# Performance work log

Measured on AMD Instinct MI355X. Metric: run time of the kernel, lower is better.

Reference implementation:

```python
import jax, jax.numpy as jnp
import numpy as np


def _gcn_layer(ann, adj, Wa, ba, W2, b2):
    # ann: [B,N,F], adj: [B,E,N,N], Wa: [E,F,U], ba: [E,U], W2: [F,U], b2: [U]
    # per-edge-type linear, fused as one batched einsum -> [B,E,N,U]
    h = jnp.einsum('bnf,efu->benu', ann, Wa) + ba[None, :, None, :]
    # adjacency matmul per edge type: [B,E,N,N] @ [B,E,N,U]
    h = jnp.einsum('benm,bemu->benu', adj, h)
    # sum over edge types + residual linear + activation (tanh)
    out = h.sum(axis=1) + jnp.einsum('bnf,fu->bnu', ann, W2) + b2
    return jnp.tanh(out)


def setup_inputs() -> dict:
    key = jax.random.key(0)
    ks = jax.random.split(key, 10)
    B, N, F, E, U = 32, 1024, 32, 4, 32
    s = 1.0 / np.sqrt(F)
    s1 = 1.0 / np.sqrt(F + U)
    return {
        'n_tensor': jax.random.normal(ks[0], (B, N, F), dtype=jnp.float32),
        'adj_tensor': jax.random.uniform(ks[1], (B, E, N, N), dtype=jnp.float32),
        'W_adj0': jax.random.normal(ks[2], (E, F, U), dtype=jnp.float32) * s,
        'b_adj0': jax.random.normal(ks[3], (E, U), dtype=jnp.float32) * s,
        'W2_0': jax.random.normal(ks[4], (F, U), dtype=jnp.float32) * s,
        'b2_0': jax.random.normal(ks[5], (U,), dtype=jnp.float32) * s,
        'W_adj1': jax.random.normal(ks[6], (E, F + U, U), dtype=jnp.float32) * s1,
        'b_adj1': jax.random.normal(ks[7], (E, U), dtype=jnp.float32) * s1,
        'W2_1': jax.random.normal(ks[8], (F + U, U), dtype=jnp.float32) * s1,
        'b2_1': jax.random.normal(ks[9], (U,), dtype=jnp.float32) * s1,
    }


def reference(n_tensor, adj_tensor, W_adj0, b_adj0, W2_0, b2_0,
              W_adj1, b_adj1, W2_1, b2_1):
    # layer 0: h_tensor is None -> annotations = n_tensor
    h = _gcn_layer(n_tensor, adj_tensor, W_adj0, b_adj0, W2_0, b2_0)
    # layer 1: annotations = cat(n_tensor, hidden)
    ann1 = jnp.concatenate([n_tensor, h], axis=-1)
    h = _gcn_layer(ann1, adj_tensor, W_adj1, b_adj1, W2_1, b2_1)
    return h
```

## Files before the change

### kernel.cpp

```cpp
#include <hip/hip_runtime.h>
#include <math.h>

#define Bb 32
#define Nn 1024
#define Ee 4
#define Uu 32

template <int F, int FA>
__global__ __launch_bounds__(128) void pre_kernel(
    const float* __restrict__ annA, const float* __restrict__ annB,
    const float* __restrict__ Wa, const float* __restrict__ ba,
    const float* __restrict__ W2, const float* __restrict__ b2,
    float* __restrict__ hpre_t, float* __restrict__ res)
{
    __shared__ float wlds[5 * F * Uu];
    __shared__ float blds[5 * Uu];
    const int tid = threadIdx.x;
    for (int i = tid; i < 4 * F * Uu; i += 128) wlds[i] = Wa[i];
    for (int i = tid; i < F * Uu; i += 128) wlds[4 * F * Uu + i] = W2[i];
    for (int i = tid; i < 4 * Uu; i += 128) blds[i] = ba[i];
    for (int i = tid; i < Uu; i += 128) blds[4 * Uu + i] = b2[i];
    __syncthreads();

    const int g = blockIdx.x * 128 + tid;
    const int b = g >> 10;
    const int n = g & 1023;

    float4 a4[F / 4];
    {
        const float4* rA = (const float4*)(annA + (size_t)g * FA);
#pragma unroll
        for (int i = 0; i < FA / 4; ++i) a4[i] = rA[i];
        if constexpr (F > FA) {
            const float4* rB = (const float4*)(annB + (size_t)g * (F - FA));
#pragma unroll
            for (int i = 0; i < (F - FA) / 4; ++i) a4[FA / 4 + i] = rB[i];
        }
    }

    for (int e = 0; e < 5; ++e) {
        float4 acc[8];
        const float4* bb = (const float4*)(blds + e * Uu);
#pragma unroll
        for (int uq = 0; uq < 8; ++uq) acc[uq] = bb[uq];
        const float4* w4 = (const float4*)wlds + (size_t)e * F * 8;
#pragma unroll
        for (int f4 = 0; f4 < F / 4; ++f4) {
            const float4 av = a4[f4];
#pragma unroll
            for (int c = 0; c < 4; ++c) {
                const float s = (c == 0) ? av.x : (c == 1) ? av.y : (c == 2) ? av.z : av.w;
#pragma unroll
                for (int uq = 0; uq < 8; ++uq) {
                    const float4 w = w4[(f4 * 4 + c) * 8 + uq];
                    acc[uq].x = fmaf(s, w.x, acc[uq].x);
                    acc[uq].y = fmaf(s, w.y, acc[uq].y);
                    acc[uq].z = fmaf(s, w.z, acc[uq].z);
                    acc[uq].w = fmaf(s, w.w, acc[uq].w);
                }
            }
        }
        if (e < 4) {
            float* dst = hpre_t + ((size_t)(b * 4 + e) * Uu) * Nn + n;
#pragma unroll
            for (int uq = 0; uq < 8; ++uq) {
                dst[(uq * 4 + 0) * Nn] = acc[uq].x;
                dst[(uq * 4 + 1) * Nn] = acc[uq].y;
                dst[(uq * 4 + 2) * Nn] = acc[uq].z;
                dst[(uq * 4 + 3) * Nn] = acc[uq].w;
            }
        } else {
            float4* dst = (float4*)(res + (size_t)g * Uu);
#pragma unroll
            for (int uq = 0; uq < 8; ++uq) dst[uq] = acc[uq];
        }
    }
}

__global__ __launch_bounds__(256) void gcn_main_kernel(
    const float* __restrict__ adj,
    const float* __restrict__ hpre_t,
    const float* __restrict__ res,
    float* __restrict__ out)
{
    __shared__ float hbuf[2][Uu * 64];

    const int bid = blockIdx.x;
    const int swz = (bid & 7) * 128 + (bid >> 3);
    const int b = swz >> 5;
    const int n0 = (swz & 31) * 32;
    const int tid = threadIdx.x;
    const int w = tid >> 6;
    const int lane = tid & 63;
    const int gu = lane >> 4;
    const int ms = lane & 15;
    const int wrow = n0 + w * 8;

    float acc[8][8];
#pragma unroll
    for (int r = 0; r < 8; ++r)
#pragma unroll
        for (int j = 0; j < 8; ++j) acc[r][j] = 0.f;

    const float* adjb = adj + (size_t)b * Ee * Nn * Nn;
    const float* hpb = hpre_t + (size_t)b * Ee * Uu * Nn;

    const int fi0 = tid, fi1 = tid + 256;
    const int su0 = fi0 >> 4, sm0 = fi0 & 15;
    const int su1 = fi1 >> 4, sm1 = fi1 & 15;

    float4 hstage0 = *(const float4*)(hpb + (size_t)su0 * Nn + sm0 * 4);
    float4 hstage1 = *(const float4*)(hpb + (size_t)su1 * Nn + sm1 * 4);

    for (int it = 0; it < 64; ++it) {
        const int e = it >> 4, c = it & 15;
        float* hb = hbuf[it & 1];

        const float* arow = adjb + ((size_t)e * Nn + wrow) * Nn + c * 64 + ms * 4;
        float4 av[8];
#pragma unroll
        for (int r = 0; r < 8; ++r) av[r] = *(const float4*)(arow + (size_t)r * Nn);

        ((float4*)hb)[fi0] = hstage0;
        ((float4*)hb)[fi1] = hstage1;

        if (it < 63) {
            const int e2 = (it + 1) >> 4, c2 = (it + 1) & 15;
            const float* hc = hpb + (size_t)e2 * Uu * Nn + c2 * 64;
            hstage0 = *(const float4*)(hc + (size_t)su0 * Nn + sm0 * 4);
            hstage1 = *(const float4*)(hc + (size_t)su1 * Nn + sm1 * 4);
        }
        __syncthreads();

#pragma unroll
        for (int j = 0; j < 8; ++j) {
            const float4 h = *(const float4*)(hb + (gu * 8 + j) * 64 + ms * 4);
#pragma unroll
            for (int r = 0; r < 8; ++r) {
                float t = fmaf(av[r].x, h.x, acc[r][j]);
                t = fmaf(av[r].y, h.y, t);
                t = fmaf(av[r].z, h.z, t);
                acc[r][j] = fmaf(av[r].w, h.w, t);
            }
        }
    }

#pragma unroll
    for (int r = 0; r < 8; ++r)
#pragma unroll
        for (int j = 0; j < 8; ++j) {
            float v = acc[r][j];
            v += __shfl_xor(v, 1);
            v += __shfl_xor(v, 2);
            v += __shfl_xor(v, 4);
            v += __shfl_xor(v, 8);
            acc[r][j] = v;
        }

#pragma unroll
    for (int r = 0; r < 8; ++r) {
        if (ms == r) {
            const int n = wrow + r;
            const float* rp = res + ((size_t)b * Nn + n) * Uu + gu * 8;
            float* op = out + ((size_t)b * Nn + n) * Uu + gu * 8;
            const float4 r0 = *(const float4*)(rp);
            const float4 r1 = *(const float4*)(rp + 4);
            float4 o0, o1;
            o0.x = tanhf(acc[r][0] + r0.x);
            o0.y = tanhf(acc[r][1] + r0.y);
            o0.z = tanhf(acc[r][2] + r0.z);
            o0.w = tanhf(acc[r][3] + r0.w);
            o1.x = tanhf(acc[r][4] + r1.x);
            o1.y = tanhf(acc[r][5] + r1.y);
            o1.z = tanhf(acc[r][6] + r1.z);
            o1.w = tanhf(acc[r][7] + r1.w);
            *(float4*)(op) = o0;
            *(float4*)(op + 4) = o1;
        }
    }
}

extern "C" void kernel_launch(void* const* d_in, const int* in_sizes, int n_in,
                              void* d_out, int out_size, void* d_ws, size_t ws_size,
                              hipStream_t stream)
{
    const float* n_tensor = (const float*)d_in[0];
    const float* adj      = (const float*)d_in[1];
    const float* W_adj0   = (const float*)d_in[2];
    const float* b_adj0   = (const float*)d_in[3];
    const float* W2_0     = (const float*)d_in[4];
    const float* b2_0     = (const float*)d_in[5];
    const float* W_adj1   = (const float*)d_in[6];
    const float* b_adj1   = (const float*)d_in[7];
    const float* W2_1     = (const float*)d_in[8];
    const float* b2_1     = (const float*)d_in[9];
    float* outp = (float*)d_out;

    float* ws   = (float*)d_ws;
    float* hpre = ws;
    float* resb = ws + (size_t)4 * 1024 * 1024;
    float* h0   = ws + (size_t)5 * 1024 * 1024;

    pre_kernel<32, 32><<<256, 128, 0, stream>>>(n_tensor, nullptr, W_adj0, b_adj0,
                                                W2_0, b2_0, hpre, resb);
    gcn_main_kernel<<<1024, 256, 0, stream>>>(adj, hpre, resb, h0);

    pre_kernel<64, 32><<<256, 128, 0, stream>>>(n_tensor, h0, W_adj1, b_adj1,
                                                W2_1, b2_1, hpre, resb);
    gcn_main_kernel<<<1024, 256, 0, stream>>>(adj, hpre, resb, outp);
}
```

Baseline: 496.3 us.

## Double-buffer adjacency loads in registers and split pre-kernel by edge type

The main GCN kernel now prefetches the next chunk's adjacency rows into an alternate register set (adjA/adjB ping-pong) while computing on the current one. It replaces __syncthreads with an explicit LDS waitcnt, a raw barrier and a sched_barrier, aiming to hide global load latency behind the FMAs. The pre-kernel is split across a second grid dimension, one block column per edge type plus the residual, with 256 threads. This gives more parallel blocks and smaller shared memory, at the cost of reloading the annotations five times. The extra adjacency register buffer raises register pressure and may reduce occupancy.

```diff
diff --git a/kernel.cpp b/kernel.cpp
--- a/kernel.cpp
+++ b/kernel.cpp
@@ -7,22 +7,23 @@
 #define Uu 32
 
 template <int F, int FA>
-__global__ __launch_bounds__(128) void pre_kernel(
+__global__ __launch_bounds__(256) void pre_kernel(
     const float* __restrict__ annA, const float* __restrict__ annB,
     const float* __restrict__ Wa, const float* __restrict__ ba,
     const float* __restrict__ W2, const float* __restrict__ b2,
     float* __restrict__ hpre_t, float* __restrict__ res)
 {
-    __shared__ float wlds[5 * F * Uu];
-    __shared__ float blds[5 * Uu];
+    const int e = blockIdx.y;
+    __shared__ float wlds[F * Uu];
+    __shared__ float blds[Uu];
     const int tid = threadIdx.x;
-    for (int i = tid; i < 4 * F * Uu; i += 128) wlds[i] = Wa[i];
-    for (int i = tid; i < F * Uu; i += 128) wlds[4 * F * Uu + i] = W2[i];
-    for (int i = tid; i < 4 * Uu; i += 128) blds[i] = ba[i];
-    for (int i = tid; i < Uu; i += 128) blds[4 * Uu + i] = b2[i];
+    const float* wsrc = (e < 4) ? (Wa + (size_t)e * F * Uu) : W2;
+    const float* bsrc = (e < 4) ? (ba + (size_t)e * Uu) : b2;
+    for (int i = tid; i < F * Uu; i += 256) wlds[i] = wsrc[i];
+    if (tid < Uu) blds[tid] = bsrc[tid];
     __syncthreads();
 
-    const int g = blockIdx.x * 128 + tid;
+    const int g = blockIdx.x * 256 + tid;
     const int b = g >> 10;
     const int n = g & 1023;
 
@@ -38,42 +39,40 @@
         }
     }
 
-    for (int e = 0; e < 5; ++e) {
-        float4 acc[8];
-        const float4* bb = (const float4*)(blds + e * Uu);
-#pragma unroll
-        for (int uq = 0; uq < 8; ++uq) acc[uq] = bb[uq];
-        const float4* w4 = (const float4*)wlds + (size_t)e * F * 8;
-#pragma unroll
-        for (int f4 = 0; f4 < F / 4; ++f4) {
-            const float4 av = a4[f4];
-#pragma unroll
-            for (int c = 0; c < 4; ++c) {
-                const float s = (c == 0) ? av.x : (c == 1) ? av.y : (c == 2) ? av.z : av.w;
-#pragma unroll
-                for (int uq = 0; uq < 8; ++uq) {
-                    const float4 w = w4[(f4 * 4 + c) * 8 + uq];
-                    acc[uq].x = fmaf(s, w.x, acc[uq].x);
-                    acc[uq].y = fmaf(s, w.y, acc[uq].y);
-                    acc[uq].z = fmaf(s, w.z, acc[uq].z);
-                    acc[uq].w = fmaf(s, w.w, acc[uq].w);
-                }
+    float4 acc[8];
+    const float4* bb = (const float4*)blds;
+#pragma unroll
+    for (int uq = 0; uq < 8; ++uq) acc[uq] = bb[uq];
+    const float4* w4 = (const float4*)wlds;
+#pragma unroll
+    for (int f4 = 0; f4 < F / 4; ++f4) {
+        const float4 av = a4[f4];
+#pragma unroll
+        for (int c = 0; c < 4; ++c) {
+            const float s = (c == 0) ? av.x : (c == 1) ? av.y : (c == 2) ? av.z : av.w;
+#pragma unroll
+            for (int uq = 0; uq < 8; ++uq) {
+                const float4 w = w4[(f4 * 4 + c) * 8 + uq];
+                acc[uq].x = fmaf(s, w.x, acc[uq].x);
+                acc[uq].y = fmaf(s, w.y, acc[uq].y);
+                acc[uq].z = fmaf(s, w.z, acc[uq].z);
+                acc[uq].w = fmaf(s, w.w, acc[uq].w);
             }
         }
-        if (e < 4) {
-            float* dst = hpre_t + ((size_t)(b * 4 + e) * Uu) * Nn + n;
-#pragma unroll
-            for (int uq = 0; uq < 8; ++uq) {
-                dst[(uq * 4 + 0) * Nn] = acc[uq].x;
-                dst[(uq * 4 + 1) * Nn] = acc[uq].y;
-                dst[(uq * 4 + 2) * Nn] = acc[uq].z;
-                dst[(uq * 4 + 3) * Nn] = acc[uq].w;
-            }
-        } else {
-            float4* dst = (float4*)(res + (size_t)g * Uu);
-#pragma unroll
-            for (int uq = 0; uq < 8; ++uq) dst[uq] = acc[uq];
-        }
+    }
+    if (e < 4) {
+        float* dst = hpre_t + ((size_t)(b * 4 + e) * Uu) * Nn + n;
+#pragma unroll
+        for (int uq = 0; uq < 8; ++uq) {
+            dst[(uq * 4 + 0) * Nn] = acc[uq].x;
+            dst[(uq * 4 + 1) * Nn] = acc[uq].y;
+            dst[(uq * 4 + 2) * Nn] = acc[uq].z;
+            dst[(uq * 4 + 3) * Nn] = acc[uq].w;
+        }
+    } else {
+        float4* dst = (float4*)(res + (size_t)g * Uu);
+#pragma unroll
+        for (int uq = 0; uq < 8; ++uq) dst[uq] = acc[uq];
     }
 }
 
@@ -109,41 +108,52 @@
     const int su0 = fi0 >> 4, sm0 = fi0 & 15;
     const int su1 = fi1 >> 4, sm1 = fi1 & 15;
 
-    float4 hstage0 = *(const float4*)(hpb + (size_t)su0 * Nn + sm0 * 4);
-    float4 hstage1 = *(const float4*)(hpb + (size_t)su1 * Nn + sm1 * 4);
-
-    for (int it = 0; it < 64; ++it) {
-        const int e = it >> 4, c = it & 15;
-        float* hb = hbuf[it & 1];
-
-        const float* arow = adjb + ((size_t)e * Nn + wrow) * Nn + c * 64 + ms * 4;
-        float4 av[8];
-#pragma unroll
-        for (int r = 0; r < 8; ++r) av[r] = *(const float4*)(arow + (size_t)r * Nn);
-
-        ((float4*)hb)[fi0] = hstage0;
-        ((float4*)hb)[fi1] = hstage1;
-
-        if (it < 63) {
-            const int e2 = (it + 1) >> 4, c2 = (it + 1) & 15;
-            const float* hc = hpb + (size_t)e2 * Uu * Nn + c2 * 64;
-            hstage0 = *(const float4*)(hc + (size_t)su0 * Nn + sm0 * 4);
-            hstage1 = *(const float4*)(hc + (size_t)su1 * Nn + sm1 * 4);
-        }
-        __syncthreads();
-
-#pragma unroll
-        for (int j = 0; j < 8; ++j) {
-            const float4 h = *(const float4*)(hb + (gu * 8 + j) * 64 + ms * 4);
-#pragma unroll
-            for (int r = 0; r < 8; ++r) {
-                float t = fmaf(av[r].x, h.x, acc[r][j]);
-                t = fmaf(av[r].y, h.y, t);
-                t = fmaf(av[r].z, h.z, t);
-                acc[r][j] = fmaf(av[r].w, h.w, t);
-            }
-        }
-    }
+    float4 adjA[8], adjB[8];
+    float4 h0, h1;
+
+    {
+        const float* ap = adjb + (size_t)wrow * Nn + ms * 4;
+#pragma unroll
+        for (int r = 0; r < 8; ++r) adjA[r] = *(const float4*)(ap + (size_t)r * Nn);
+        h0 = *(const float4*)(hpb + (size_t)su0 * Nn + sm0 * 4);
+        h1 = *(const float4*)(hpb + (size_t)su1 * Nn + sm1 * 4);
+    }
+
+#define GCN_BODY(CUR, ALT, T)                                                   \
+    {                                                                           \
+        const int t_ = (T);                                                     \
+        float* hb = hbuf[t_ & 1];                                               \
+        ((float4*)hb)[fi0] = h0;                  \
+        ((float4*)hb)[fi1] = h1;                                                \
+        const int tn_ = (t_ < 63) ? t_ + 1 : 63;                                \
+        const int e2_ = tn_ >> 4, c2_ = tn_ & 15;                               \
+        const float* ap_ = adjb + ((size_t)e2_ * Nn + wrow) * Nn + c2_ * 64 + ms * 4; \
+        _Pragma("unroll")                                                       \
+        for (int r = 0; r < 8; ++r) ALT[r] = *(const float4*)(ap_ + (size_t)r * Nn); \
+        const float* hc_ = hpb + (size_t)e2_ * Uu * Nn + c2_ * 64;              \
+        h0 = *(const float4*)(hc_ + (size_t)su0 * Nn + sm0 * 4);                \
+        h1 = *(const float4*)(hc_ + (size_t)su1 * Nn + sm1 * 4);                \
+        asm volatile("s_waitcnt lgkmcnt(0)" ::: "memory");                      \
+        __builtin_amdgcn_s_barrier();                                           \
+        __builtin_amdgcn_sched_barrier(0);                                      \
+        _Pragma("unroll")                                                       \
+        for (int j = 0; j < 8; ++j) {                                           \
+            const float4 hv = *(const float4*)(hb + (gu * 8 + j) * 64 + ms * 4); \
+            _Pragma("unroll")                                                   \
+            for (int r = 0; r < 8; ++r) {                                       \
+                float t = fmaf(CUR[r].x, hv.x, acc[r][j]);                      \
+                t = fmaf(CUR[r].y, hv.y, t);                                    \
+                t = fmaf(CUR[r].z, hv.z, t);                                    \
+                acc[r][j] = fmaf(CUR[r].w, hv.w, t);                            \
+            }                                                                   \
+        }                                                                       \
+    }
+
+    for (int t = 0; t < 64; t += 2) {
+        GCN_BODY(adjA, adjB, t);
+        GCN_BODY(adjB, adjA, t + 1);
+    }
+#undef GCN_BODY
 
 #pragma unroll
     for (int r = 0; r < 8; ++r)
@@ -201,11 +211,13 @@
     float* resb = ws + (size_t)4 * 1024 * 1024;
     float* h0   = ws + (size_t)5 * 1024 * 1024;
 
-    pre_kernel<32, 32><<<256, 128, 0, stream>>>(n_tensor, nullptr, W_adj0, b_adj0,
-                                                W2_0, b2_0, hpre, resb);
+    dim3 pre_grid(128, 5);
+
+    pre_kernel<32, 32><<<pre_grid, 256, 0, stream>>>(n_tensor, nullptr, W_adj0, b_adj0,
+                                                     W2_0, b2_0, hpre, resb);
     gcn_main_kernel<<<1024, 256, 0, stream>>>(adj, hpre, resb, h0);
 
-    pre_kernel<64, 32><<<256, 128, 0, stream>>>(n_tensor, h0, W_adj1, b_adj1,
-                                                W2_1, b2_1, hpre, resb);
+    pre_kernel<64, 32><<<pre_grid, 256, 0, stream>>>(n_tensor, h0, W_adj1, b_adj1,
+                                                     W2_1, b2_1, hpre, resb);
     gcn_main_kernel<<<1024, 256, 0, stream>>>(adj, hpre, resb, outp);
 }
```

New measurement: 426.9 us. 14.0% less time.
